# Performance work log

Measured on AMD Instinct MI355X. Metric: run time of the kernel, lower is better.

Reference implementation:

```python
import jax, jax.numpy as jnp
import numpy as np
from jax import lax

# Module config (matches init_kwargs)
B, CIN, COUT, H, W = 64, 128, 256, 64, 64
K, STRIDE, PAD = 4, 2, 1
POOL_K, POOL_S = 2, 2
HT_MIN, HT_MAX = -1.0, 1.0


def setup_inputs() -> dict:
    key = jax.random.key(0)
    k1, k2, k3 = jax.random.split(key, 3)
    x = jax.random.normal(k1, (B, CIN, H, W), dtype=jnp.float32)
    # torch ConvTranspose2d default init scale ~ 1/sqrt(Cin*K*K)
    scale = 1.0 / np.sqrt(CIN * K * K)
    weight = jax.random.normal(k2, (CIN, COUT, K, K), dtype=jnp.float32) * scale
    bias = jax.random.normal(k3, (COUT,), dtype=jnp.float32) * scale
    return {"x": x, "weight": weight, "bias": bias}


def reference(x, weight, bias):
    # ConvTranspose2d(stride=2, padding=1): equivalent forward conv with
    # lhs_dilation=stride, flipped kernel, padding k-1-p on each side.
    w = jnp.flip(weight, axis=(2, 3)).transpose(1, 0, 2, 3)  # (Cout, Cin, K, K)
    pad = K - 1 - PAD
    y = lax.conv_general_dilated(
        x, w,
        window_strides=(1, 1),
        padding=[(pad, pad), (pad, pad)],
        lhs_dilation=(STRIDE, STRIDE),
        dimension_numbers=("NCHW", "OIHW", "NCHW"),
    ) + bias[None, :, None, None]  # [B, Cout, 128, 128]

    # MaxPool2d(kernel=2, stride=2), VALID
    y = lax.reduce_window(
        y, -jnp.inf, lax.max,
        window_dimensions=(1, 1, POOL_K, POOL_K),
        window_strides=(1, 1, POOL_S, POOL_S),
        padding="VALID",
    )  # [B, Cout, 64, 64]

    # Hardtanh -> spatial mean (keepdim) -> Tanh
    y = jnp.clip(y, HT_MIN, HT_MAX)
    y = jnp.mean(y, axis=(2, 3), keepdims=True)  # [B, Cout, 1, 1]
    return jnp.tanh(y)
```

## Files before the change

kernel.cpp:

```cpp
#include <hip/hip_runtime.h>
#include <hip/hip_bf16.h>
#include <cstdint>


typedef __attribute__((ext_vector_type(8))) short short8;
typedef __attribute__((ext_vector_type(4))) float f32x4;

#define SWZ 1

__device__ __forceinline__ void async16(const void* g, void* l) {
  __builtin_amdgcn_global_load_lds(
      reinterpret_cast<const unsigned int __attribute__((address_space(1)))*>(
          reinterpret_cast<uintptr_t>(g)),
      reinterpret_cast<unsigned int __attribute__((address_space(3)))*>(
          reinterpret_cast<uintptr_t>(l)),
      16, 0, 0);
}

__device__ __forceinline__ unsigned short f2bf(float f) {
  union { float f; unsigned int u; } v; v.f = f;
  unsigned int u = v.u;
  return (unsigned short)((u + 0x7fffu + ((u >> 16) & 1u)) >> 16);
}

__global__ __launch_bounds__(256) void k_xpose(const float* __restrict__ x,
                                               unsigned short* __restrict__ xT) {
  __shared__ float tile[64][132];
  int bid = blockIdx.x;
  int b = bid >> 6, h = bid & 63;
  const float* src = x + (size_t)b * 524288 + h * 64;
  int w = threadIdx.x & 63, cg = threadIdx.x >> 6;
#pragma unroll
  for (int cc = 0; cc < 32; ++cc) {
    int cin = cc * 4 + cg;
    tile[w][cin] = src[(size_t)cin * 4096 + w];
  }
  __syncthreads();
  unsigned short* dst = xT + (size_t)(b * 64 + h) * 8192;
#pragma unroll
  for (int it = 0; it < 4; ++it) {
    int e = it * 2048 + threadIdx.x * 8;
    int ww = e >> 7, cin = e & 127;
    unsigned int pk[4];
#pragma unroll
    for (int j = 0; j < 4; ++j) {
      unsigned int lo = f2bf(tile[ww][cin + 2 * j]);
      unsigned int hi = f2bf(tile[ww][cin + 2 * j + 1]);
      pk[j] = lo | (hi << 16);
    }
    *reinterpret_cast<uint4*>(dst + e) = make_uint4(pk[0], pk[1], pk[2], pk[3]);
  }
}

__global__ __launch_bounds__(256) void k_wpack(const float* __restrict__ w,
                                               unsigned short* __restrict__ wT) {
  int o = blockIdx.x * 256 + threadIdx.x;
  int cin = o & 127;
  int cout = (o >> 7) & 255;
  int khkw = o >> 15;
  int kh = khkw >> 2, kw = khkw & 3;
  float f = w[((size_t)cin * 256 + cout) * 16 + kh * 4 + kw];
  wT[o] = f2bf(f);
}

#define XROW_B   16896
#define WBUF0_B  67584
#define WBUF_SZ  32768
#define LDS_TOTAL 133120

__global__ __launch_bounds__(256, 1) void k_main(
    const unsigned short* __restrict__ xT,
    const unsigned short* __restrict__ wT,
    const float* __restrict__ bias,
    float* __restrict__ acc) {
  extern __shared__ char smem[];
  const int bid = blockIdx.x;
  const int nt = bid & 1;
  const int pr = (bid >> 1) & 31;
  const int b  = bid >> 6;
  const int n0 = nt * 128;
  const int tid = threadIdx.x;
  const int lane = tid & 63;
  const int wid = tid >> 6;
  const int wm = wid >> 1;
  const int wn = wid & 1;
  const int l15 = lane & 15;
  const int l4  = lane >> 4;

  {
    const int r = wid;
    const int ir = 2 * pr - 1 + r;
    char* rowbase = smem + r * XROW_B;
    f32x4 z = {0.f, 0.f, 0.f, 0.f};
    if ((unsigned)ir < 64u) {
      const char* g0 = (const char*)xT + (size_t)(b * 64 + ir) * 16384;
#pragma unroll
      for (int it = 0; it < 16; ++it) {
        int c = 1 + it * 4 + l4;
#if SWZ
        int key = ((r * 66 + c) & 7) << 4;
#else
        int key = 0;
#endif
        const char* srcp = g0 + (c - 1) * 256 + ((l15 * 16) ^ key);
        async16(srcp, rowbase + 256 + it * 1024);
      }
      if (lane < 16)       *reinterpret_cast<f32x4*>(rowbase + lane * 16) = z;
      else if (lane < 32)  *reinterpret_cast<f32x4*>(rowbase + 65 * 256 + (lane - 16) * 16) = z;
    } else {
#pragma unroll
      for (int it = 0; it < 17; ++it) {
        int off = it * 1024 + lane * 16;
        if (off < XROW_B) *reinterpret_cast<f32x4*>(rowbase + off) = z;
      }
    }
  }

  auto stage_w = [&](int khkw, int buf) {
    char* dst = smem + WBUF0_B + buf * WBUF_SZ + wid * 8192;
    const char* g0 = (const char*)wT + ((size_t)khkw * 256 + n0) * 256;
#pragma unroll
    for (int it = 0; it < 8; ++it) {
      int cl = wid * 32 + it * 4 + l4;
#if SWZ
      int key = (cl & 7) << 4;
#else
      int key = 0;
#endif
      async16(g0 + cl * 256 + ((l15 * 16) ^ key), dst + it * 1024);
    }
  };

  const int KHt[2][2] = {{1, 3}, {2, 0}};
  const int DHt[2][2] = {{0, -1}, {0, 1}};

  stage_w(5, 0);
  __syncthreads();

  f32x4 accf[4][4], rm[4][4];
#pragma unroll
  for (int mi = 0; mi < 4; ++mi)
#pragma unroll
    for (int ni = 0; ni < 4; ++ni) accf[mi][ni] = (f32x4){0.f, 0.f, 0.f, 0.f};

  unsigned boff[4]; int bkey[4];
#pragma unroll
  for (int ni = 0; ni < 4; ++ni) {
    int cl = wn * 64 + ni * 16 + l15;
    boff[ni] = cl * 256 + l4 * 16;
#if SWZ
    bkey[ni] = (cl & 7) << 4;
#else
    bkey[ni] = 0;
#endif
  }

#pragma unroll
  for (int q = 0; q < 4; ++q) {
    const int qh = q >> 1, qw = q & 1;
#pragma unroll
    for (int t = 0; t < 4; ++t) {
      const int th = t >> 1, tw = t & 1;
      const int idx = q * 4 + t;
      if (idx < 15) {
        const int nidx = idx + 1;
        const int q2 = nidx >> 2, t2 = nidx & 3;
        const int kh2 = KHt[q2 >> 1][t2 >> 1];
        const int kw2 = KHt[q2 & 1][t2 & 1];
        stage_w(kh2 * 4 + kw2, nidx & 1);
      }
      const int ar = wm + 1 + DHt[qh][th];
      const int dw = DHt[qw][tw];
      unsigned aoff[4]; int akey[4];
#pragma unroll
      for (int mi = 0; mi < 4; ++mi) {
        int c = 1 + mi * 16 + l15 + dw;
        int rowi = ar * 66 + c;
        aoff[mi] = rowi * 256 + l4 * 16;
#if SWZ
        akey[mi] = (rowi & 7) << 4;
#else
        akey[mi] = 0;
#endif
      }
      char* wb = smem + WBUF0_B + (idx & 1) * WBUF_SZ;
#pragma unroll
      for (int kk = 0; kk < 4; ++kk) {
        short8 a[4], bb[4];
#pragma unroll
        for (int mi = 0; mi < 4; ++mi)
          a[mi] = *reinterpret_cast<const short8*>(smem + ((aoff[mi] + kk * 64) ^ akey[mi]));
#pragma unroll
        for (int ni = 0; ni < 4; ++ni)
          bb[ni] = *reinterpret_cast<const short8*>(wb + ((boff[ni] + kk * 64) ^ bkey[ni]));
#pragma unroll
        for (int mi = 0; mi < 4; ++mi)
#pragma unroll
          for (int ni = 0; ni < 4; ++ni)
            accf[mi][ni] = __builtin_amdgcn_mfma_f32_16x16x32_bf16(a[mi], bb[ni], accf[mi][ni], 0, 0, 0);
      }
      if (t == 3) {
#pragma unroll
        for (int mi = 0; mi < 4; ++mi)
#pragma unroll
          for (int ni = 0; ni < 4; ++ni) {
            if (q == 0) {
              rm[mi][ni] = accf[mi][ni];
            } else {
#pragma unroll
              for (int rr = 0; rr < 4; ++rr)
                rm[mi][ni][rr] = fmaxf(rm[mi][ni][rr], accf[mi][ni][rr]);
            }
            accf[mi][ni] = (f32x4){0.f, 0.f, 0.f, 0.f};
          }
      }
      __syncthreads();
    }
  }

#pragma unroll
  for (int ni = 0; ni < 4; ++ni) {
    const int cout = n0 + wn * 64 + ni * 16 + l15;
    const float bv = bias[cout];
    float s = 0.f;
#pragma unroll
    for (int mi = 0; mi < 4; ++mi)
#pragma unroll
      for (int rr = 0; rr < 4; ++rr) {
        float v = rm[mi][ni][rr] + bv;
        v = fminf(1.f, fmaxf(-1.f, v));
        s += v;
      }
    s += __shfl_xor(s, 16, 64);
    s += __shfl_xor(s, 32, 64);
    if (lane < 16) atomicAdd(&acc[b * 256 + cout], s);
  }
}

__global__ __launch_bounds__(256) void k_fin(const float* __restrict__ acc,
                                             float* __restrict__ out) {
  int i = blockIdx.x * 256 + threadIdx.x;
  out[i] = tanhf(acc[i] * (1.0f / 4096.0f));
}

extern "C" void kernel_launch(void* const* d_in, const int* in_sizes, int n_in,
                              void* d_out, int out_size, void* d_ws, size_t ws_size,
                              hipStream_t stream) {
  const float* x    = (const float*)d_in[0];
  const float* w    = (const float*)d_in[1];
  const float* bias = (const float*)d_in[2];
  float* out = (float*)d_out;
  char* ws = (char*)d_ws;

  float* acc          = (float*)ws;
  unsigned short* xT  = (unsigned short*)(ws + 65536);
  unsigned short* wT  = (unsigned short*)(ws + 65536 + 67108864);

  hipMemsetAsync(acc, 0, 65536, stream);
  k_xpose<<<4096, 256, 0, stream>>>(x, xT);
  k_wpack<<<2048, 256, 0, stream>>>(w, wT);

  hipFuncSetAttribute(reinterpret_cast<const void*>(k_main),
                      hipFuncAttributeMaxDynamicSharedMemorySize, LDS_TOTAL);
  k_main<<<4096, 256, LDS_TOTAL, stream>>>(xT, wT, bias, acc);
  k_fin<<<64, 256, 0, stream>>>(acc, out);
}
```

Baseline: 347.8 us.

## Double block size to share weight tiles across two pooled rows

The main kernel now runs 512-thread blocks. Each block stages six input rows and covers two pooled output rows, so each staged weight tile feeds eight waves instead of four, which halves weight LDS staging and global traffic per output. The zero-padding columns in the LDS input layout are dropped: edge columns are clamped and then masked to zero in registers. This also doubles resident waves per CU, giving more latency hiding. The cost is a larger LDS footprint and a tighter register budget under launch_bounds(512,2), which could cause spills.

Result: slower. 424.6 us (+22.1%).

```diff
diff --git a/kernel.cpp b/kernel.cpp
--- a/kernel.cpp
+++ b/kernel.cpp
@@ -5,8 +5,6 @@
 
 typedef __attribute__((ext_vector_type(8))) short short8;
 typedef __attribute__((ext_vector_type(4))) float f32x4;
-
-#define SWZ 1
 
 __device__ __forceinline__ void async16(const void* g, void* l) {
   __builtin_amdgcn_global_load_lds(
@@ -21,6 +19,13 @@
   union { float f; unsigned int u; } v; v.f = f;
   unsigned int u = v.u;
   return (unsigned short)((u + 0x7fffu + ((u >> 16) & 1u)) >> 16);
+}
+
+__device__ __forceinline__ short8 and_mask(short8 v, unsigned m) {
+  union { short8 s; unsigned u[4]; } x;
+  x.s = v;
+  x.u[0] &= m; x.u[1] &= m; x.u[2] &= m; x.u[3] &= m;
+  return x.s;
 }
 
 __global__ __launch_bounds__(256) void k_xpose(const float* __restrict__ x,
@@ -63,76 +68,65 @@
   wT[o] = f2bf(f);
 }
 
-#define XROW_B   16896
-#define WBUF0_B  67584
+#define XS_B     98304
 #define WBUF_SZ  32768
-#define LDS_TOTAL 133120
-
-__global__ __launch_bounds__(256, 1) void k_main(
+#define LDS_TOTAL 163840
+
+__global__ __launch_bounds__(512, 2) void k_main(
     const unsigned short* __restrict__ xT,
     const unsigned short* __restrict__ wT,
     const float* __restrict__ bias,
     float* __restrict__ acc) {
   extern __shared__ char smem[];
   const int bid = blockIdx.x;
-  const int nt = bid & 1;
-  const int pr = (bid >> 1) & 31;
-  const int b  = bid >> 6;
-  const int n0 = nt * 128;
-  const int tid = threadIdx.x;
+  const int nt  = bid & 1;
+  const int prg = (bid >> 1) & 15;
+  const int b   = bid >> 5;
+  const int n0  = nt * 128;
+  const int tid  = threadIdx.x;
   const int lane = tid & 63;
-  const int wid = tid >> 6;
-  const int wm = wid >> 1;
-  const int wn = wid & 1;
-  const int l15 = lane & 15;
-  const int l4  = lane >> 4;
+  const int wid  = tid >> 6;
+  const int wm   = wid >> 1;
+  const int wn   = wid & 1;
+  const int l15  = lane & 15;
 
   {
-    const int r = wid;
-    const int ir = 2 * pr - 1 + r;
-    char* rowbase = smem + r * XROW_B;
-    f32x4 z = {0.f, 0.f, 0.f, 0.f};
-    if ((unsigned)ir < 64u) {
-      const char* g0 = (const char*)xT + (size_t)(b * 64 + ir) * 16384;
-#pragma unroll
-      for (int it = 0; it < 16; ++it) {
-        int c = 1 + it * 4 + l4;
-#if SWZ
-        int key = ((r * 66 + c) & 7) << 4;
-#else
-        int key = 0;
-#endif
-        const char* srcp = g0 + (c - 1) * 256 + ((l15 * 16) ^ key);
-        async16(srcp, rowbase + 256 + it * 1024);
-      }
-      if (lane < 16)       *reinterpret_cast<f32x4*>(rowbase + lane * 16) = z;
-      else if (lane < 32)  *reinterpret_cast<f32x4*>(rowbase + 65 * 256 + (lane - 16) * 16) = z;
-    } else {
-#pragma unroll
-      for (int it = 0; it < 17; ++it) {
-        int off = it * 1024 + lane * 16;
-        if (off < XROW_B) *reinterpret_cast<f32x4*>(rowbase + off) = z;
+    const char* xTb = (const char*)xT + (size_t)b * 1048576;
+#pragma unroll
+    for (int it = 0; it < 12; ++it) {
+      const int gbase = wid * 12288 + it * 1024;
+      const int g = gbase + lane * 16;
+      const int r = g >> 14;
+      const int ir = 4 * prg - 1 + r;
+      const int rc = g >> 8;
+      const int key = (rc & 7) << 4;
+      if ((unsigned)ir < 64u) {
+        const int oir = g & 16383;
+        const char* src = xTb + ir * 16384 + (oir & ~255) + ((oir & 255) ^ key);
+        async16(src, smem + gbase);
+      } else {
+        *reinterpret_cast<f32x4*>(smem + g) = (f32x4){0.f, 0.f, 0.f, 0.f};
       }
     }
   }
 
   auto stage_w = [&](int khkw, int buf) {
-    char* dst = smem + WBUF0_B + buf * WBUF_SZ + wid * 8192;
+    char* dstbase = smem + XS_B + buf * WBUF_SZ;
     const char* g0 = (const char*)wT + ((size_t)khkw * 256 + n0) * 256;
 #pragma unroll
-    for (int it = 0; it < 8; ++it) {
-      int cl = wid * 32 + it * 4 + l4;
-#if SWZ
-      int key = (cl & 7) << 4;
-#else
-      int key = 0;
-#endif
-      async16(g0 + cl * 256 + ((l15 * 16) ^ key), dst + it * 1024);
+    for (int it = 0; it < 4; ++it) {
+      const int gbase = wid * 4096 + it * 1024;
+      const int g = gbase + lane * 16;
+      const int cl = g >> 8;
+      const int key = (cl & 7) << 4;
+      async16(g0 + (g & ~255) + ((g & 255) ^ key), dstbase + gbase);
     }
   };
 
   const int KHt[2][2] = {{1, 3}, {2, 0}};
   const int DHt[2][2] = {{0, -1}, {0, 1}};
+  const unsigned kmneg = (l15 == 0)  ? 0u : ~0u;
+  const unsigned kmpos = (l15 == 15) ? 0u : ~0u;
 
   stage_w(5, 0);
   __syncthreads();
@@ -147,12 +141,8 @@
 #pragma unroll
   for (int ni = 0; ni < 4; ++ni) {
     int cl = wn * 64 + ni * 16 + l15;
-    boff[ni] = cl * 256 + l4 * 16;
-#if SWZ
+    boff[ni] = cl * 256 + (lane >> 4) * 16;
     bkey[ni] = (cl & 7) << 4;
-#else
-    bkey[ni] = 0;
-#endif
   }
 
 #pragma unroll
@@ -169,27 +159,27 @@
         const int kw2 = KHt[q2 & 1][t2 & 1];
         stage_w(kh2 * 4 + kw2, nidx & 1);
       }
-      const int ar = wm + 1 + DHt[qh][th];
+      const int dr = DHt[qh][th];
       const int dw = DHt[qw][tw];
+      const int ar = wm + 1 + dr;
       unsigned aoff[4]; int akey[4];
 #pragma unroll
       for (int mi = 0; mi < 4; ++mi) {
-        int c = 1 + mi * 16 + l15 + dw;
-        int rowi = ar * 66 + c;
-        aoff[mi] = rowi * 256 + l4 * 16;
-#if SWZ
-        akey[mi] = (rowi & 7) << 4;
-#else
-        akey[mi] = 0;
-#endif
-      }
-      char* wb = smem + WBUF0_B + (idx & 1) * WBUF_SZ;
+        int col = mi * 16 + l15 + dw;
+        int colc = col < 0 ? 0 : (col > 63 ? 63 : col);
+        int rc = ar * 64 + colc;
+        aoff[mi] = rc * 256 + (lane >> 4) * 16;
+        akey[mi] = (rc & 7) << 4;
+      }
+      char* wb = smem + XS_B + (idx & 1) * WBUF_SZ;
 #pragma unroll
       for (int kk = 0; kk < 4; ++kk) {
         short8 a[4], bb[4];
 #pragma unroll
         for (int mi = 0; mi < 4; ++mi)
           a[mi] = *reinterpret_cast<const short8*>(smem + ((aoff[mi] + kk * 64) ^ akey[mi]));
+        if (dw < 0) a[0] = and_mask(a[0], kmneg);
+        if (dw > 0) a[3] = and_mask(a[3], kmpos);
 #pragma unroll
         for (int ni = 0; ni < 4; ++ni)
           bb[ni] = *reinterpret_cast<const short8*>(wb + ((boff[ni] + kk * 64) ^ bkey[ni]));
@@ -262,6 +252,6 @@
 
   hipFuncSetAttribute(reinterpret_cast<const void*>(k_main),
                       hipFuncAttributeMaxDynamicSharedMemorySize, LDS_TOTAL);
-  k_main<<<4096, 256, LDS_TOTAL, stream>>>(xT, wT, bias, acc);
+  k_main<<<2048, 512, LDS_TOTAL, stream>>>(xT, wT, bias, acc);
   k_fin<<<64, 256, 0, stream>>>(acc, out);
 }
```
